# Kernel optimization log

Hardware: AMD Instinct MI355X
Metric: run time of the kernel (lower is better)

The kernel has to match this reference:

```python
import jax, jax.numpy as jnp
import numpy as np
from functools import partial

TAU_MEM = 10.0
TAU_SYN = (5.0, 10.0)
THRESHOLD = 1.0
WINDOW = 0.3
BATCH = 32
T = 256
N_SYN = 2
N_NEURONS = 2048


@jax.custom_vjp
def spike_fn(v_shifted):
    # Heaviside of (vmem - threshold); surrogate gradient is a boxcar of width `window`.
    return (v_shifted > 0).astype(v_shifted.dtype)


def _spike_fwd(v_shifted):
    return spike_fn(v_shifted), v_shifted


def _spike_bwd(v_shifted, g):
    surr = (jnp.abs(v_shifted) < WINDOW).astype(g.dtype) / WINDOW
    return (g * surr,)


spike_fn.defvjp(_spike_fwd, _spike_bwd)


def setup_inputs() -> dict:
    key = jax.random.key(0)
    # Poisson-like analog spike input, shape (batch*T, n_syn, n_neurons)
    binary_input = (jax.random.uniform(key, (BATCH * T, N_SYN, N_NEURONS), dtype=jnp.float32) < 0.1
                    ).astype(jnp.float32)
    return {"binary_input": binary_input}


def reference(binary_input):
    # (B*T, n_syn, N) -> (B, T, n_syn, N) -> time-major, synapse-last: (T, B, N, n_syn)
    x = binary_input.reshape(BATCH, T, N_SYN, N_NEURONS).transpose(1, 0, 3, 2)

    alpha_mem = jnp.exp(jnp.float32(-1.0 / TAU_MEM))
    alpha_syn = jnp.exp(-1.0 / jnp.asarray(TAU_SYN, dtype=jnp.float32))  # [n_syn]

    def step(carry, inp_t):
        vmem, isyn = carry                      # vmem [B,N], isyn [B,N,n_syn]
        isyn = alpha_syn * isyn + inp_t         # leaky synaptic integration
        vmem = alpha_mem * vmem + isyn.sum(-1)  # leaky membrane integration
        spikes = spike_fn(vmem - THRESHOLD)     # threshold crossing
        vmem = vmem - spikes * THRESHOLD        # reset by subtraction
        return (vmem, isyn), spikes

    v0 = jnp.zeros((BATCH, N_NEURONS), dtype=x.dtype)
    i0 = jnp.zeros((BATCH, N_NEURONS, N_SYN), dtype=x.dtype)
    _, all_spikes = jax.lax.scan(step, (v0, i0), x)  # [T, B, N]

    # back to (batch*T, N) as in the torch module's trailing reshape
    return all_spikes.transpose(1, 0, 2).reshape(-1, N_NEURONS)
```

## Files before the change

kernel.cpp:

```cpp
#include <hip/hip_runtime.h>
#include <math.h>

#define T_STEPS   256
#define N_NEUR    2048
#define N_BATCH   32

__global__ __launch_bounds__(256) void snn_scan_kernel(
    const float* __restrict__ in,
    float* __restrict__ out,
    float a_mem, float a_s0, float a_s1)
{
    const int tid = blockIdx.x * blockDim.x + threadIdx.x;
    const int n = tid & (N_NEUR - 1);
    const int b = tid >> 11;

    const float* pin = in + (size_t)b * T_STEPS * 2 * N_NEUR + n;
    float* pout      = out + (size_t)b * T_STEPS * N_NEUR + n;

    float vmem = 0.0f;
    float i0 = 0.0f;
    float i1 = 0.0f;

    #pragma unroll 8
    for (int t = 0; t < T_STEPS; ++t) {
        const float x0 = pin[(size_t)t * (2 * N_NEUR)];
        const float x1 = pin[(size_t)t * (2 * N_NEUR) + N_NEUR];

        i0 = __fadd_rn(__fmul_rn(a_s0, i0), x0);
        i1 = __fadd_rn(__fmul_rn(a_s1, i1), x1);

        const float ssum = __fadd_rn(i0, i1);
        vmem = __fadd_rn(__fmul_rn(a_mem, vmem), ssum);

        const float vs = __fsub_rn(vmem, 1.0f);
        const bool fired = (vs > 0.0f);
        const float spike = fired ? 1.0f : 0.0f;
        vmem = fired ? vs : vmem;

        pout[(size_t)t * N_NEUR] = spike;
    }
}

extern "C" void kernel_launch(void* const* d_in, const int* in_sizes, int n_in,
                              void* d_out, int out_size, void* d_ws, size_t ws_size,
                              hipStream_t stream) {
    const float* in = (const float*)d_in[0];
    float* out = (float*)d_out;

    const float a_s0  = (float)exp((double)(-1.0f / 5.0f));
    const float a_s1  = (float)exp((double)(-1.0f / 10.0f));
    const float a_mem = (float)exp((double)(-1.0f / 10.0f));

    const int total_threads = N_BATCH * N_NEUR;
    dim3 block(256);
    dim3 grid(total_threads / 256);

    snn_scan_kernel<<<grid, block, 0, stream>>>(in, out, a_mem, a_s0, a_s1);
}
```

Measured before the change: 208.2 us.

## Double-buffer input loads in register chunks to overlap memory with the scan

Restructures the time loop into 16-step chunks and keeps two register buffers. While one chunk is being computed, the loads for the next chunk are already in flight. The goal is to hide global-memory latency on the serial recurrence by keeping more loads outstanding per thread. In exchange it uses more registers (64 floats of buffers), which could lower occupancy.

```diff
diff --git a/kernel.cpp b/kernel.cpp
--- a/kernel.cpp
+++ b/kernel.cpp
@@ -4,6 +4,10 @@
 #define T_STEPS   256
 #define N_NEUR    2048
 #define N_BATCH   32
+
+#define CHUNK   16
+#define NCHUNK  (T_STEPS / CHUNK)
+
 
 __global__ __launch_bounds__(256) void snn_scan_kernel(
     const float* __restrict__ in,
@@ -21,24 +25,47 @@
     float i0 = 0.0f;
     float i1 = 0.0f;
 
-    #pragma unroll 8
-    for (int t = 0; t < T_STEPS; ++t) {
-        const float x0 = pin[(size_t)t * (2 * N_NEUR)];
-        const float x1 = pin[(size_t)t * (2 * N_NEUR) + N_NEUR];
+    float xa0[CHUNK], xb0[CHUNK];
+    float xa1[CHUNK], xb1[CHUNK];
 
-        i0 = __fadd_rn(__fmul_rn(a_s0, i0), x0);
-        i1 = __fadd_rn(__fmul_rn(a_s1, i1), x1);
+#define LOADC(XA, XB, CIDX)                                                  \
+    {                                                                        \
+        const float* p_ = pin + (size_t)(CIDX) * CHUNK * (2 * N_NEUR);       \
+        _Pragma("unroll")                                                    \
+        for (int k = 0; k < CHUNK; ++k) {                                    \
+            XA[k] = p_[(size_t)k * (2 * N_NEUR)];                            \
+            XB[k] = p_[(size_t)k * (2 * N_NEUR) + N_NEUR];                   \
+        }                                                                    \
+    }
 
-        const float ssum = __fadd_rn(i0, i1);
-        vmem = __fadd_rn(__fmul_rn(a_mem, vmem), ssum);
+#define COMPUTEC(XA, XB, CIDX)                                               \
+    {                                                                        \
+        float* po_ = pout + (size_t)(CIDX) * CHUNK * N_NEUR;                 \
+        _Pragma("unroll")                                                    \
+        for (int k = 0; k < CHUNK; ++k) {                                    \
+            i0 = __fadd_rn(__fmul_rn(a_s0, i0), XA[k]);                      \
+            i1 = __fadd_rn(__fmul_rn(a_s1, i1), XB[k]);                      \
+            const float ssum = __fadd_rn(i0, i1);                            \
+            vmem = __fadd_rn(__fmul_rn(a_mem, vmem), ssum);                  \
+            const float vs = __fsub_rn(vmem, 1.0f);                          \
+            const bool fired = (vs > 0.0f);                                  \
+            po_[(size_t)k * N_NEUR] = fired ? 1.0f : 0.0f;                   \
+            vmem = fired ? vs : vmem;                                        \
+        }                                                                    \
+    }
 
-        const float vs = __fsub_rn(vmem, 1.0f);
-        const bool fired = (vs > 0.0f);
-        const float spike = fired ? 1.0f : 0.0f;
-        vmem = fired ? vs : vmem;
+    LOADC(xa0, xb0, 0);
+    LOADC(xa1, xb1, 1);
 
-        pout[(size_t)t * N_NEUR] = spike;
+    for (int c = 0; c < NCHUNK; c += 2) {
+        COMPUTEC(xa0, xb0, c);
+        if (c + 2 < NCHUNK) LOADC(xa0, xb0, c + 2);
+        COMPUTEC(xa1, xb1, c + 1);
+        if (c + 3 < NCHUNK) LOADC(xa1, xb1, c + 3);
     }
+
+#undef LOADC
+#undef COMPUTEC
 }
 
 extern "C" void kernel_launch(void* const* d_in, const int* in_sizes, int n_in,
```

Result: no change. 211.4 us (+1.5%).
